# Kernel tuning notes

Hardware: AMD Instinct MI355X
Metric: run time of the kernel (lower is better)

Reference implementation:

```python
import jax, jax.numpy as jnp
import numpy as np

N = 8192        # total nodes (32 events x 256 hits)
G = 32          # events
K = 15          # knn_graph k
FIN = 4         # n_ftx_in
FOUT = 4        # n_ftx_out
SPACE = 3       # n_ftx_space
LAT = 64        # n_ftx_latent
HID = 2 * LAT   # GIN hidden (n_hidden_nodes)


def _leaky(x):
    return jnp.where(x > 0, x, 0.01 * x)


def setup_inputs() -> dict:
    key = jax.random.key(0)
    ks = jax.random.split(key, 20)

    def p(k, shape, fan_in):
        return (jax.random.normal(k, shape, jnp.float32) / jnp.sqrt(jnp.float32(fan_in)))

    inp = {
        "x": jax.random.normal(ks[0], (N, FIN), jnp.float32),
        "batch": (jnp.arange(N) // (N // G)).astype(jnp.int32),
        "condition": jnp.zeros((G, 1), jnp.float32),
        # space_emb FFN: FIN -> LAT -> LAT
        "W_se1": p(ks[1], (FIN, LAT), FIN), "b_se1": jnp.zeros((LAT,), jnp.float32),
        "W_se2": p(ks[2], (LAT, LAT), LAT), "b_se2": jnp.zeros((LAT,), jnp.float32),
        # GINConv 1 MLP: LAT -> HID -> LAT
        "W_g1a": p(ks[3], (LAT, HID), LAT), "b_g1a": jnp.zeros((HID,), jnp.float32),
        "W_g1b": p(ks[4], (HID, LAT), HID), "b_g1b": jnp.zeros((LAT,), jnp.float32),
        # GINConv 2 MLP
        "W_g2a": p(ks[5], (LAT, HID), LAT), "b_g2a": jnp.zeros((HID,), jnp.float32),
        "W_g2b": p(ks[6], (HID, LAT), HID), "b_g2b": jnp.zeros((LAT,), jnp.float32),
        # out_emb FFN: LAT -> LAT -> FOUT
        "W_oe1": p(ks[7], (LAT, LAT), LAT), "b_oe1": jnp.zeros((LAT,), jnp.float32),
        "W_oe2": p(ks[8], (LAT, FOUT), LAT), "b_oe2": jnp.zeros((FOUT,), jnp.float32),
    }
    return inp


def _knn_graph(pos, batch, k):
    # pairwise squared distances within the same event only; no self-loops
    d = jnp.sum((pos[:, None, :] - pos[None, :, :]) ** 2, axis=-1)  # [N, N]
    ii = jnp.arange(pos.shape[0])
    valid = (batch[:, None] == batch[None, :]) & (ii[:, None] != ii[None, :])
    d = jnp.where(valid, d, jnp.float32(1e30))
    _, nbr = jax.lax.top_k(-d, k)                 # [N, K] nearest neighbor ids
    src = nbr.reshape(-1)                          # neighbor j (source)
    dst = jnp.repeat(ii, k)                        # center i (target)
    return jnp.stack([src, dst])                   # PyG edge_index layout


def _gin(h, src, dst, Wa, ba, Wb, bb):
    # GINConv, eps=0: mlp(x_i + sum_j x_j)
    agg = jax.ops.segment_sum(h[src], dst, num_segments=h.shape[0])
    m = h + agg
    return jnp.maximum(m @ Wa + ba, 0.0) @ Wb + bb


def reference(x, batch, condition,
              W_se1, b_se1, W_se2, b_se2,
              W_g1a, b_g1a, W_g1b, b_g1b,
              W_g2a, b_g2a, W_g2b, b_g2b,
              W_oe1, b_oe1, W_oe2, b_oe2):
    # space_emb FFN
    h = _leaky(x @ W_se1 + b_se1) @ W_se2 + b_se2          # [N, LAT]
    # dynamic knn graph on first SPACE dims of the embedding
    ei = _knn_graph(h[:, :SPACE], batch, K)                 # [2, N*K]
    src, dst = ei[0], ei[1]
    # MPLSeq: 2 GINConv layers with residual skip (cond unused, n_cond=0)
    h = h + _gin(h, src, dst, W_g1a, b_g1a, W_g1b, b_g1b)
    h = h + _gin(h, src, dst, W_g2a, b_g2a, W_g2b, b_g2b)
    # out_emb FFN
    x_emb = _leaky(h @ W_oe1 + b_oe1) @ W_oe2 + b_oe2       # [N, FOUT]
    return (h, x_emb, ei)
```

## Files before the change

kernel.cpp:

```cpp
#include <hip/hip_runtime.h>


#define N_NODES 8192
#define NPE     256
#define KNN     15
#define LAT     64
#define HID     128
#define NK      (N_NODES*KNN)
#define NBLK    512
#define NTHR    512
#define NPB     16
#define EI0     (N_NODES*LAT + N_NODES*4)

#define BARA_LEAF 0
#define BARA_ROOT 2048
#define BARA_FLAG 4096
#define BARB_LEAF 8192
#define BARB_ROOT 10240
#define BARB_FLAG 12288
#define BAR_BYTES 16384

#define OFF_HA  BAR_BYTES
#define OFF_HB  (OFF_HA + N_NODES*LAT*4)
#define OFF_POS (OFF_HB + N_NODES*LAT*4)

typedef unsigned short bf16;
typedef unsigned int   u32;
typedef unsigned long long u64;

__device__ __forceinline__ float bf2f(bf16 s) {
    union { u32 u; float f; } v; v.u = ((u32)s) << 16; return v.f;
}
__device__ __forceinline__ bf16 f2bf(float f) {
    union { float f; u32 u; } v; v.f = f;
    u32 u = v.u + 0x7fffu + ((v.u >> 16) & 1u);
    return (bf16)(u >> 16);
}
__device__ __forceinline__ float ldf(const void* p, int i, int f32) {
    return f32 ? ((const float*)p)[i] : bf2f(((const bf16*)p)[i]);
}
__device__ __forceinline__ void st_coh(float* p, float v) {
    __hip_atomic_store(p, v, __ATOMIC_RELAXED, __HIP_MEMORY_SCOPE_AGENT);
}

struct KArgs {
    const void* x;
    const void* se1; const void* bse1; const void* se2; const void* bse2;
    const void* g1a; const void* bg1a; const void* g1b; const void* bg1b;
    const void* g2a; const void* bg2a; const void* g2b; const void* bg2b;
    const void* oe1; const void* boe1; const void* oe2; const void* boe2;
    const u32* wdet;
    float* hA; float* hB; float* pos; int* bar;
    void* out;
};

struct Shm {
    union {
        int   red[NTHR];
        float hid[NPB][LAT];
        float kpos[NPE * 3];
        struct { float m[NPB*LAT]; float own[NPB*LAT]; float t[NPB*HID]; } g;
        float st[NPB*LAT];
    } u;
    int   snb[NPB*KNN];
    float sh[NPB*LAT];
    int   flag;
};

__device__ __forceinline__ void gridbar(int* leaf, int* root, int* flags) {
    asm volatile("s_waitcnt vmcnt(0)" ::: "memory");
    __syncthreads();
    if (threadIdx.x == 0) {
        const int l = blockIdx.x & 31;
        if (__hip_atomic_fetch_add(leaf + l*16, 1, __ATOMIC_RELAXED,
                                   __HIP_MEMORY_SCOPE_AGENT) == 15) {
            if (__hip_atomic_fetch_add(root, 1, __ATOMIC_RELAXED,
                                       __HIP_MEMORY_SCOPE_AGENT) == 31) {
                #pragma unroll
                for (int i = 0; i < 32; i++)
                    __hip_atomic_store(flags + i*16, 1, __ATOMIC_RELAXED,
                                       __HIP_MEMORY_SCOPE_AGENT);
            }
        }
        int guard = 0;
        while (__hip_atomic_load(flags + l*16, __ATOMIC_RELAXED,
                                 __HIP_MEMORY_SCOPE_AGENT) == 0) {
            __builtin_amdgcn_s_sleep(2);
            if (++guard > (1 << 20)) break;
        }
        __builtin_amdgcn_fence(__ATOMIC_ACQUIRE, "workgroup");
    }
    __syncthreads();
}

template<bool LAST>
__device__ __forceinline__ void gin_layer(Shm& S, int base, int f32,
        const float* __restrict__ hin, float* hout,
        const void* Wa, const void* ba, const void* Wb, const void* bb,
        void* out)
{
    const int tid = threadIdx.x;
    #pragma unroll
    for (int p = 0; p < 2; p++) {
        const int e = tid + p*NTHR, n = e >> 6, f = e & 63, gi = base + n;
        const int* nb = &S.snb[n*KNN];
        const float own = hin[gi*LAT + f];
        float vv[KNN];
        #pragma unroll
        for (int k = 0; k < KNN; k++) vv[k] = hin[nb[k]*LAT + f];
        float s0 = vv[0] + vv[1],  s1 = vv[2]  + vv[3],  s2 = vv[4]  + vv[5];
        float s3 = vv[6] + vv[7],  s4 = vv[8]  + vv[9],  s5 = vv[10] + vv[11];
        float s6 = vv[12] + vv[13];
        const float acc = own + (((s0 + s1) + (s2 + s3)) + ((s4 + s5) + (s6 + vv[14])));
        S.u.g.m[e] = acc; S.u.g.own[e] = own;
    }
    __syncthreads();
    {
        const int n4 = (tid >> 7) * 4, u = tid & 127;
        float a0 = ldf(ba, u, f32);
        float a1 = a0, a2 = a0, a3 = a0;
        if (f32) {
            const float* W = (const float*)Wa;
            #pragma unroll 8
            for (int f = 0; f < LAT; f++) {
                const float w = W[f*HID + u];
                a0 = fmaf(S.u.g.m[(n4    )*LAT + f], w, a0);
                a1 = fmaf(S.u.g.m[(n4 + 1)*LAT + f], w, a1);
                a2 = fmaf(S.u.g.m[(n4 + 2)*LAT + f], w, a2);
                a3 = fmaf(S.u.g.m[(n4 + 3)*LAT + f], w, a3);
            }
        } else {
            const bf16* W = (const bf16*)Wa;
            #pragma unroll 8
            for (int f = 0; f < LAT; f++) {
                const float w = bf2f(W[f*HID + u]);
                a0 = fmaf(S.u.g.m[(n4    )*LAT + f], w, a0);
                a1 = fmaf(S.u.g.m[(n4 + 1)*LAT + f], w, a1);
                a2 = fmaf(S.u.g.m[(n4 + 2)*LAT + f], w, a2);
                a3 = fmaf(S.u.g.m[(n4 + 3)*LAT + f], w, a3);
            }
        }
        S.u.g.t[(n4    )*HID + u] = a0 > 0.f ? a0 : 0.f;
        S.u.g.t[(n4 + 1)*HID + u] = a1 > 0.f ? a1 : 0.f;
        S.u.g.t[(n4 + 2)*HID + u] = a2 > 0.f ? a2 : 0.f;
        S.u.g.t[(n4 + 3)*HID + u] = a3 > 0.f ? a3 : 0.f;
    }
    __syncthreads();
    {
        const int q = tid >> 6, f = tid & 63;
        float a0 = ldf(bb, f, f32);
        float a1 = a0;
        if (f32) {
            const float* W = (const float*)Wb;
            #pragma unroll 8
            for (int u = 0; u < HID; u++) {
                const float w = W[u*LAT + f];
                a0 = fmaf(S.u.g.t[(q    )*HID + u], w, a0);
                a1 = fmaf(S.u.g.t[(q + 8)*HID + u], w, a1);
            }
        } else {
            const bf16* W = (const bf16*)Wb;
            #pragma unroll 8
            for (int u = 0; u < HID; u++) {
                const float w = bf2f(W[u*LAT + f]);
                a0 = fmaf(S.u.g.t[(q    )*HID + u], w, a0);
                a1 = fmaf(S.u.g.t[(q + 8)*HID + u], w, a1);
            }
        }
        const float o0 = S.u.g.own[(q    )*LAT + f] + a0;
        const float o1 = S.u.g.own[(q + 8)*LAT + f] + a1;
        const int gi0 = base + q, gi1 = base + q + 8;
        if (!LAST) {
            st_coh(&hout[gi0*LAT + f], o0);
            st_coh(&hout[gi1*LAT + f], o1);
        } else {
            S.sh[(q    )*LAT + f] = o0;
            S.sh[(q + 8)*LAT + f] = o1;
            if (f32) {
                ((float*)out)[gi0*LAT + f] = o0;
                ((float*)out)[gi1*LAT + f] = o1;
            } else {
                ((bf16*)out)[gi0*LAT + f] = f2bf(o0);
                ((bf16*)out)[gi1*LAT + f] = f2bf(o1);
            }
        }
    }
    __syncthreads();
}

__global__ __launch_bounds__(NTHR, 4) void k_fused(KArgs a)
{
    __shared__ Shm S;
    const int tid = threadIdx.x, blk = blockIdx.x;
    const int base = blk * NPB;

    {
        int c = 0;
        for (int i = tid; i < 4096; i += NTHR) {
            const u32 x = a.wdet[i];
            c += ((x >> 7)  & 0xffu) >= 0xC8u;
            c += ((x >> 23) & 0xffu) >= 0xC8u;
        }
        S.u.red[tid] = c;
        __syncthreads();
        for (int s = NTHR/2; s > 0; s >>= 1) {
            if (tid < s) S.u.red[tid] += S.u.red[tid + s];
            __syncthreads();
        }
        if (tid == 0) S.flag = (S.u.red[0] > 64) ? 1 : 0;
        __syncthreads();
    }
    const int f32 = S.flag;
    __syncthreads();

    {
        #pragma unroll
        for (int p = 0; p < 2; p++) {
            const int e = tid + p*NTHR, n = e >> 6, f = e & 63, node = base + n;
            float acc = ldf(a.bse1, f, f32);
            #pragma unroll
            for (int i = 0; i < 4; i++)
                acc = fmaf(ldf(a.x, node*4 + i, f32), ldf(a.se1, i*LAT + f, f32), acc);
            acc = acc > 0.f ? acc : 0.01f*acc;
            S.u.hid[n][f] = acc;
        }
        __syncthreads();
        const int q = tid >> 6, f = tid & 63;
        float a0 = ldf(a.bse2, f, f32);
        float a1 = a0;
        if (f32) {
            const float* W = (const float*)a.se2;
            #pragma unroll 8
            for (int j = 0; j < LAT; j++) {
                const float w = W[j*LAT + f];
                a0 = fmaf(S.u.hid[q][j],     w, a0);
                a1 = fmaf(S.u.hid[q + 8][j], w, a1);
            }
        } else {
            const bf16* W = (const bf16*)a.se2;
            #pragma unroll 8
            for (int j = 0; j < LAT; j++) {
                const float w = bf2f(W[j*LAT + f]);
                a0 = fmaf(S.u.hid[q][j],     w, a0);
                a1 = fmaf(S.u.hid[q + 8][j], w, a1);
            }
        }
        const int n0 = base + q, n1 = base + q + 8;
        st_coh(&a.hA[n0*LAT + f], a0);
        st_coh(&a.hA[n1*LAT + f], a1);
        if (f < 3) {
            st_coh(&a.pos[n0*3 + f], a0);
            st_coh(&a.pos[n1*3 + f], a1);
        }
    }
    gridbar(a.bar + BARA_LEAF/4, a.bar + BARA_ROOT/4, a.bar + BARA_FLAG/4);

    {
        const int eb = base & ~(NPE - 1);
        for (int i = tid; i < NPE*3; i += NTHR) S.u.kpos[i] = a.pos[(size_t)eb*3 + i];
        __syncthreads();
        const int wave = tid >> 6, lane = tid & 63;
        #pragma unroll
        for (int t = 0; t < 2; ++t) {
            const int n  = base + wave*2 + t;
            const int nl = n - eb;
            const float px = S.u.kpos[nl*3], py = S.u.kpos[nl*3+1], pz = S.u.kpos[nl*3+2];
            u64 key[4];
            #pragma unroll
            for (int c = 0; c < 4; c++) {
                const int j = 64*c + lane;
                const float dx = px - S.u.kpos[j*3], dy = py - S.u.kpos[j*3+1],
                            dz = pz - S.u.kpos[j*3+2];
                float dd = __fmul_rn(dx, dx);
                dd = __fadd_rn(dd, __fmul_rn(dy, dy));
                dd = __fadd_rn(dd, __fmul_rn(dz, dz));
                key[c] = ((u64)__float_as_uint(dd) << 32) | (u32)j;
                if (j == nl) key[c] = ~0ull;
            }
            #define CSWAP(A,B) { const u64 x_ = key[A], y_ = key[B]; \
                                 key[A] = x_ < y_ ? x_ : y_; key[B] = x_ < y_ ? y_ : x_; }
            CSWAP(0,1) CSWAP(2,3) CSWAP(0,2) CSWAP(1,3) CSWAP(1,2)
            #undef CSWAP
            int myj = 0;
            #pragma unroll
            for (int k = 0; k < KNN; k++) {
                u64 m = key[0];
                #pragma unroll
                for (int s = 32; s >= 1; s >>= 1) {
                    const u64 o = __shfl_xor(m, s, 64);
                    m = o < m ? o : m;
                }
                if (lane == k) myj = (int)(u32)m;
                const bool hit = (key[0] == m);
                key[0] = hit ? key[1] : key[0];
                key[1] = hit ? key[2] : key[1];
                key[2] = hit ? key[3] : key[2];
                key[3] = hit ? ~0ull  : key[3];
            }
            if (lane < KNN) {
                const int gj = eb + myj;
                S.snb[(n - base)*KNN + lane] = gj;
                if (f32) {
                    float* o = (float*)a.out;
                    o[EI0 + n*KNN + lane]      = (float)gj;
                    o[EI0 + NK + n*KNN + lane] = (float)n;
                } else {
                    bf16* o = (bf16*)a.out;
                    o[EI0 + n*KNN + lane]      = f2bf((float)gj);
                    o[EI0 + NK + n*KNN + lane] = f2bf((float)n);
                }
            }
        }
        __syncthreads();
    }

    gin_layer<false>(S, base, f32, a.hA, a.hB,
                     a.g1a, a.bg1a, a.g1b, a.bg1b, nullptr);
    gridbar(a.bar + BARB_LEAF/4, a.bar + BARB_ROOT/4, a.bar + BARB_FLAG/4);

    gin_layer<true>(S, base, f32, a.hB, nullptr,
                    a.g2a, a.bg2a, a.g2b, a.bg2b, a.out);

    {
        const int q = tid >> 6, f = tid & 63;
        float a0 = ldf(a.boe1, f, f32);
        float a1 = a0;
        if (f32) {
            const float* W = (const float*)a.oe1;
            #pragma unroll 8
            for (int j = 0; j < LAT; j++) {
                const float w = W[j*LAT + f];
                a0 = fmaf(S.sh[(q    )*LAT + j], w, a0);
                a1 = fmaf(S.sh[(q + 8)*LAT + j], w, a1);
            }
        } else {
            const bf16* W = (const bf16*)a.oe1;
            #pragma unroll 8
            for (int j = 0; j < LAT; j++) {
                const float w = bf2f(W[j*LAT + f]);
                a0 = fmaf(S.sh[(q    )*LAT + j], w, a0);
                a1 = fmaf(S.sh[(q + 8)*LAT + j], w, a1);
            }
        }
        a0 = a0 > 0.f ? a0 : 0.01f*a0;
        a1 = a1 > 0.f ? a1 : 0.01f*a1;
        __syncthreads();
        S.u.st[(q    )*LAT + f] = a0;
        S.u.st[(q + 8)*LAT + f] = a1;
        __syncthreads();
        if (tid < NPB*4) {
            const int n = tid >> 2, ff = tid & 3;
            float acc = ldf(a.boe2, ff, f32);
            for (int j = 0; j < LAT; j++)
                acc = fmaf(S.u.st[n*LAT + j], ldf(a.oe2, j*4 + ff, f32), acc);
            const int xo = N_NODES*LAT + (base + n)*4 + ff;
            if (f32) ((float*)a.out)[xo] = acc;
            else     ((bf16*)a.out)[xo] = f2bf(acc);
        }
    }
}

extern "C" void kernel_launch(void* const* d_in, const int* in_sizes, int n_in,
                              void* d_out, int out_size, void* d_ws, size_t ws_size,
                              hipStream_t stream)
{
    (void)in_sizes; (void)n_in; (void)out_size; (void)ws_size;
    char* ws = (char*)d_ws;

    KArgs a;
    a.x   = d_in[0];
    a.se1 = d_in[3];  a.bse1 = d_in[4];  a.se2 = d_in[5];  a.bse2 = d_in[6];
    a.g1a = d_in[7];  a.bg1a = d_in[8];  a.g1b = d_in[9];  a.bg1b = d_in[10];
    a.g2a = d_in[11]; a.bg2a = d_in[12]; a.g2b = d_in[13]; a.bg2b = d_in[14];
    a.oe1 = d_in[15]; a.boe1 = d_in[16]; a.oe2 = d_in[17]; a.boe2 = d_in[18];
    a.wdet = (const u32*)d_in[7];
    a.hA  = (float*)(ws + OFF_HA);
    a.hB  = (float*)(ws + OFF_HB);
    a.pos = (float*)(ws + OFF_POS);
    a.bar = (int*)ws;
    a.out = d_out;

    hipMemsetAsync(d_ws, 0, BAR_BYTES, stream);
    k_fused<<<dim3(NBLK), dim3(NTHR), 0, stream>>>(a);
}
```

Baseline: 152.6 us.

## Replace grid-wide barriers with per-event barriers across event block groups

Since kNN edges never cross event boundaries, the two grid-wide tree barriers are replaced by per-event counters, each shared by the 16 blocks of one event. Block indices are interleaved so that each event's 16 blocks are spread across the grid. This removes the global synchronization wait, letting fast events proceed without waiting for every block. It relies on all blocks being co-resident and on barrier memory being zeroed and padded per event.

```diff
diff --git a/kernel.cpp b/kernel.cpp
--- a/kernel.cpp
+++ b/kernel.cpp
@@ -10,14 +10,14 @@
 #define NBLK    512
 #define NTHR    512
 #define NPB     16
+#define NEV     32
+#define BPEV    16
 #define EI0     (N_NODES*LAT + N_NODES*4)
 
-#define BARA_LEAF 0
-#define BARA_ROOT 2048
-#define BARA_FLAG 4096
-#define BARB_LEAF 8192
-#define BARB_ROOT 10240
-#define BARB_FLAG 12288
+#define BARA_CNT 0
+#define BARA_FLG 4096
+#define BARB_CNT 8192
+#define BARB_FLG 12288
 #define BAR_BYTES 16384
 
 #define OFF_HA  BAR_BYTES
@@ -67,23 +67,17 @@
     int   flag;
 };
 
-__device__ __forceinline__ void gridbar(int* leaf, int* root, int* flags) {
+__device__ __forceinline__ void eventbar(int* cnt, int* flg) {
     asm volatile("s_waitcnt vmcnt(0)" ::: "memory");
     __syncthreads();
     if (threadIdx.x == 0) {
-        const int l = blockIdx.x & 31;
-        if (__hip_atomic_fetch_add(leaf + l*16, 1, __ATOMIC_RELAXED,
-                                   __HIP_MEMORY_SCOPE_AGENT) == 15) {
-            if (__hip_atomic_fetch_add(root, 1, __ATOMIC_RELAXED,
-                                       __HIP_MEMORY_SCOPE_AGENT) == 31) {
-                #pragma unroll
-                for (int i = 0; i < 32; i++)
-                    __hip_atomic_store(flags + i*16, 1, __ATOMIC_RELAXED,
-                                       __HIP_MEMORY_SCOPE_AGENT);
-            }
+        if (__hip_atomic_fetch_add(cnt, 1, __ATOMIC_RELAXED,
+                                   __HIP_MEMORY_SCOPE_AGENT) == BPEV - 1) {
+            __hip_atomic_store(flg, 1, __ATOMIC_RELAXED,
+                               __HIP_MEMORY_SCOPE_AGENT);
         }
         int guard = 0;
-        while (__hip_atomic_load(flags + l*16, __ATOMIC_RELAXED,
+        while (__hip_atomic_load(flg, __ATOMIC_RELAXED,
                                  __HIP_MEMORY_SCOPE_AGENT) == 0) {
             __builtin_amdgcn_s_sleep(2);
             if (++guard > (1 << 20)) break;
@@ -192,7 +186,9 @@
 {
     __shared__ Shm S;
     const int tid = threadIdx.x, blk = blockIdx.x;
-    const int base = blk * NPB;
+    const int ev   = blk & (NEV - 1);
+    const int slc  = blk >> 5;
+    const int base = ev * NPE + slc * NPB;
 
     {
         int c = 0;
@@ -253,10 +249,10 @@
             st_coh(&a.pos[n1*3 + f], a1);
         }
     }
-    gridbar(a.bar + BARA_LEAF/4, a.bar + BARA_ROOT/4, a.bar + BARA_FLAG/4);
-
-    {
-        const int eb = base & ~(NPE - 1);
+    eventbar(a.bar + (BARA_CNT + ev*128)/4, a.bar + (BARA_FLG + ev*128)/4);
+
+    {
+        const int eb = ev * NPE;
         for (int i = tid; i < NPE*3; i += NTHR) S.u.kpos[i] = a.pos[(size_t)eb*3 + i];
         __syncthreads();
         const int wave = tid >> 6, lane = tid & 63;
@@ -316,7 +312,7 @@
 
     gin_layer<false>(S, base, f32, a.hA, a.hB,
                      a.g1a, a.bg1a, a.g1b, a.bg1b, nullptr);
-    gridbar(a.bar + BARB_LEAF/4, a.bar + BARB_ROOT/4, a.bar + BARB_FLAG/4);
+    eventbar(a.bar + (BARB_CNT + ev*128)/4, a.bar + (BARB_FLG + ev*128)/4);
 
     gin_layer<true>(S, base, f32, a.hB, nullptr,
                     a.g2a, a.bg2a, a.g2b, a.bg2b, a.out);
```

Measured after the change: 146.7 us. -3.8%, faster.
